# Kernel tuning notes

Hardware: AMD Instinct MI355X
Metric: run time of the kernel (lower is better)

The kernel has to match this reference:

```python
import math
import jax, jax.numpy as jnp
from jax import lax
import numpy as np

LIDAR_MAX_X = 32.0
LIDAR_MAX_Y = 32.0
NQ = 1280  # eval-branch num_queries hardcoded in the torch module


def sineembed(pos, hidden_dim=256):
    # pos (..., 2) -> (..., hidden_dim); DAB-DETR sine embedding
    half = hidden_dim // 2
    dim_t = 10000.0 ** (2.0 * (jnp.arange(half) // 2).astype(jnp.float32) / half)
    scale = 2.0 * math.pi
    px = (pos[..., 0] * scale)[..., None] / dim_t
    py = (pos[..., 1] * scale)[..., None] / dim_t

    def interleave(p):
        s = jnp.stack([jnp.sin(p[..., 0::2]), jnp.cos(p[..., 1::2])], axis=-1)
        return s.reshape(s.shape[:-2] + (-1,))

    return jnp.concatenate([interleave(py), interleave(px)], axis=-1)


def grid_sample_bilinear_zeros(value, grid):
    # value (B,C,H,W); grid (B,Hg,Wg,2) in [-1,1], (x,y) order,
    # bilinear, padding_mode='zeros', align_corners=False
    B, C, H, W = value.shape
    Hg, Wg = grid.shape[1], grid.shape[2]
    gx = ((grid[..., 0] + 1.0) * 0.5 * W - 0.5).reshape(B, -1)
    gy = ((grid[..., 1] + 1.0) * 0.5 * H - 0.5).reshape(B, -1)
    x0 = jnp.floor(gx)
    y0 = jnp.floor(gy)
    wx1 = gx - x0
    wy1 = gy - y0
    vflat = value.reshape(B, C, H * W)

    def gather(ix, iy, w):
        valid = (ix >= 0) & (ix <= W - 1) & (iy >= 0) & (iy <= H - 1)
        ixc = jnp.clip(ix, 0, W - 1).astype(jnp.int32)
        iyc = jnp.clip(iy, 0, H - 1).astype(jnp.int32)
        idx = iyc * W + ixc  # (B,N)
        v = jnp.take_along_axis(vflat, idx[:, None, :], axis=2)  # (B,C,N)
        return v * (w * valid)[:, None, :]

    out = (gather(x0, y0, (1 - wx1) * (1 - wy1))
           + gather(x0 + 1, y0, wx1 * (1 - wy1))
           + gather(x0, y0 + 1, (1 - wx1) * wy1)
           + gather(x0 + 1, y0 + 1, wx1 * wy1))
    return out.reshape(B, C, Hg, Wg)


def setup_inputs() -> dict:
    key = jax.random.key(0)
    ks = jax.random.split(key, 12)
    B, D, Cin, H, W = 8, 256, 64, 200, 200
    return {
        "queries": jax.random.normal(ks[0], (B, NQ, D), jnp.float32),
        "navi_points": jax.random.normal(ks[1], (B, 2), jnp.float32) * 10.0,
        "bev_feature": jax.random.normal(ks[2], (B, Cin, H, W), jnp.float32),
        "spatial_shape": jnp.array([H, W], jnp.int32),
        "point_score": jax.random.uniform(ks[3], (B, 2), jnp.float32),
        "aw_w": jax.random.normal(ks[4], (1, D), jnp.float32) * 0.02,
        "aw_b": jnp.zeros((1,), jnp.float32),
        "aws_w": jax.random.normal(ks[5], (1, D), jnp.float32) * 0.02,
        "aws_b": jnp.zeros((1,), jnp.float32),
        "conv_w": jax.random.normal(ks[6], (256, Cin, 3, 3), jnp.float32) * 0.02,
        "conv_b": jnp.zeros((256,), jnp.float32),
        "out_w": jax.random.normal(ks[7], (D, D), jnp.float32) * 0.02,
        "out_b": jnp.zeros((D,), jnp.float32),
    }


def reference(queries, navi_points, bev_feature, spatial_shape, point_score,
              aw_w, aw_b, aws_w, aws_b, conv_w, conv_b, out_w, out_b):
    B, nq, D = queries.shape
    # eval branch: expand navi_points to (B, 1280, 1, 2)
    pts = jnp.broadcast_to(navi_points.reshape(B, 1, 1, 2), (B, NQ, 1, 2))
    # normalize then swap -> grid (x=pts_y/max_x, y=pts_x/max_y)
    grid = jnp.stack([pts[..., 1] / LIDAR_MAX_X, pts[..., 0] / LIDAR_MAX_Y], axis=-1)

    # attention weights from queries, softmax over num_points (=1)
    aw = jax.nn.softmax(queries @ aw_w.T + aw_b, axis=-1)  # (B,NQ,1)

    # score weights from sine embedding of point_score
    ps = jnp.broadcast_to(point_score.reshape(B, 1, 1, 2), (B, NQ, 1, 2))
    aws = (sineembed(ps) @ aws_w.T + aws_b).reshape(B, NQ, 1)  # (B,NQ,1)

    # value projection: Conv2d 64->256, 3x3, pad 1, ReLU
    value = lax.conv_general_dilated(bev_feature, conv_w, (1, 1), 'SAME',
                                     dimension_numbers=('NCHW', 'OIHW', 'NCHW'))
    value = jax.nn.relu(value + conv_b[None, :, None, None])

    sampled = grid_sample_bilinear_zeros(value, grid)  # (B,256,NQ,1)

    out = (aw[:, None] * sampled * aws[:, None]).sum(axis=-1)  # (B,256,NQ)
    out = out.transpose(0, 2, 1)  # (B,NQ,256)
    out = out @ out_w.T + out_b
    return out + queries  # dropout is identity at inference
```

## Files before the change

kernel.cpp:

```cpp
#include <hip/hip_runtime.h>
#include <math.h>

#define NQ   1280
#define DD   256
#define CIN  64
#define HH   200
#define WW   200
#define BB   8
#define KW   576
#define TPB  256

typedef float floatx4 __attribute__((ext_vector_type(4)));

__device__ __forceinline__ float wave_reduce(float v) {
#pragma unroll
    for (int off = 32; off > 0; off >>= 1) v += __shfl_down(v, off, 64);
    return v;
}

__global__ __launch_bounds__(256) void conv_sample_kernel(
    const float* __restrict__ navi,
    const float* __restrict__ bev,
    const float* __restrict__ pscore,
    const float* __restrict__ aws_w,
    const float* __restrict__ aws_b,
    const float* __restrict__ conv_w,
    const float* __restrict__ conv_b,
    float* __restrict__ s_out,
    float* __restrict__ aws_out)
{
    const int b    = blockIdx.x >> 6;
    const int cgp  = blockIdx.x & 63;
    const int tid  = threadIdx.x;
    const int lane = tid & 63;
    const int wave = tid >> 6;

    __shared__ float win[CIN * 16];
    __shared__ float red[DD];

    float nx = navi[b * 2 + 0];
    float ny = navi[b * 2 + 1];
    float gx = (ny * (1.0f / 32.0f) + 1.0f) * 0.5f * (float)WW - 0.5f;
    float gy = (nx * (1.0f / 32.0f) + 1.0f) * 0.5f * (float)HH - 0.5f;
    float x0f = floorf(gx), y0f = floorf(gy);
    float wx1 = gx - x0f, wy1 = gy - y0f;
    int x0 = (int)x0f, y0 = (int)y0f;

    float cw[4];
    {
        float wx[2] = {1.0f - wx1, wx1};
        float wy[2] = {1.0f - wy1, wy1};
#pragma unroll
        for (int k = 0; k < 4; ++k) {
            int dx = k & 1, dy = k >> 1;
            float ixf = x0f + (float)dx, iyf = y0f + (float)dy;
            bool valid = (ixf >= 0.0f) && (ixf <= (float)(WW - 1)) &&
                         (iyf >= 0.0f) && (iyf <= (float)(HH - 1));
            cw[k] = wx[dx] * wy[dy] * (valid ? 1.0f : 0.0f);
        }
    }

    for (int idx = tid; idx < CIN * 16; idx += TPB) {
        int ci = idx >> 4, pos = idx & 15;
        int yy = y0 - 1 + (pos >> 2);
        int xx = x0 - 1 + (pos & 3);
        float v = 0.0f;
        if (yy >= 0 && yy < HH && xx >= 0 && xx < WW)
            v = bev[((size_t)b * CIN + ci) * (HH * WW) + (size_t)yy * WW + xx];
        win[idx] = v;
    }
    __syncthreads();

    const int c = cgp * 4 + wave;
    const float* wp = conv_w + (size_t)c * KW;
    float a0 = 0.f, a1 = 0.f, a2 = 0.f, a3 = 0.f;
#pragma unroll
    for (int i = 0; i < 9; ++i) {
        int k  = i * 64 + lane;
        int ci = k / 9;
        int r  = k - ci * 9;
        int ky = r / 3;
        int kx = r - ky * 3;
        int base = ci * 16 + ky * 4 + kx;
        float w = wp[k];
        a0 = fmaf(w, win[base],     a0);
        a1 = fmaf(w, win[base + 1], a1);
        a2 = fmaf(w, win[base + 4], a2);
        a3 = fmaf(w, win[base + 5], a3);
    }
    a0 = wave_reduce(a0);
    a1 = wave_reduce(a1);
    a2 = wave_reduce(a2);
    a3 = wave_reduce(a3);
    if (lane == 0) {
        float cb = conv_b[c];
        float v0 = fmaxf(a0 + cb, 0.0f);
        float v1 = fmaxf(a1 + cb, 0.0f);
        float v2 = fmaxf(a2 + cb, 0.0f);
        float v3 = fmaxf(a3 + cb, 0.0f);
        s_out[b * DD + c] = cw[0] * v0 + cw[1] * v1 + cw[2] * v2 + cw[3] * v3;
    }

    if (cgp == 0) {
        float psx = pscore[b * 2 + 0];
        float psy = pscore[b * 2 + 1];
        float p = (tid < 128) ? psy : psx;
        int j = (tid & 127) >> 1;
        float dimt = powf(10000.0f, (float)j * (1.0f / 64.0f));
        float arg = p * 6.283185307179586f / dimt;
        float e = (tid & 1) ? cosf(arg) : sinf(arg);
        red[tid] = e * aws_w[tid];
        __syncthreads();
        for (int off = 128; off > 0; off >>= 1) {
            if (tid < off) red[tid] += red[tid + off];
            __syncthreads();
        }
        if (tid == 0) aws_out[b] = red[0] + aws_b[0];
    }
}

__global__ __launch_bounds__(256) void matvec_kernel(
    const float* __restrict__ out_w,
    const float* __restrict__ out_b,
    const float* __restrict__ s_in,
    const float* __restrict__ aws_in,
    float* __restrict__ t_out)
{
    const int b    = blockIdx.x >> 6;
    const int cgp  = blockIdx.x & 63;
    const int tid  = threadIdx.x;
    const int lane = tid & 63;
    const int wave = tid >> 6;

    __shared__ float s_sh[DD];
    s_sh[tid] = s_in[b * DD + tid];
    __syncthreads();

    const int d = cgp * 4 + wave;
    const float* wp = out_w + (size_t)d * DD;
    float sum = 0.0f;
#pragma unroll
    for (int i = 0; i < 4; ++i)
        sum = fmaf(wp[i * 64 + lane], s_sh[i * 64 + lane], sum);
    sum = wave_reduce(sum);
    if (lane == 0) t_out[b * DD + d] = aws_in[b] * sum + out_b[d];
}

__global__ __launch_bounds__(256) void add_kernel(
    const floatx4* __restrict__ q4,
    const floatx4* __restrict__ t4,
    floatx4* __restrict__ out4)
{
    const int i = blockIdx.x * TPB + threadIdx.x;
    floatx4 v = __builtin_nontemporal_load(&q4[i]);
    const int b  = i / (NQ * DD / 4);
    const int d4 = i & (DD / 4 - 1);
    floatx4 tv = t4[b * (DD / 4) + d4];
    v += tv;
    __builtin_nontemporal_store(v, &out4[i]);
}

extern "C" void kernel_launch(void* const* d_in, const int* in_sizes, int n_in,
                              void* d_out, int out_size, void* d_ws, size_t ws_size,
                              hipStream_t stream) {
    const float* queries = (const float*)d_in[0];
    const float* navi    = (const float*)d_in[1];
    const float* bev     = (const float*)d_in[2];
    const float* pscore  = (const float*)d_in[4];
    const float* aws_w   = (const float*)d_in[7];
    const float* aws_b   = (const float*)d_in[8];
    const float* conv_w  = (const float*)d_in[9];
    const float* conv_b  = (const float*)d_in[10];
    const float* out_w   = (const float*)d_in[11];
    const float* out_b   = (const float*)d_in[12];

    float* s   = (float*)d_ws;
    float* aws = s + BB * DD;
    float* t   = s + BB * DD + 256;

    conv_sample_kernel<<<BB * 64, TPB, 0, stream>>>(navi, bev, pscore, aws_w,
                                                    aws_b, conv_w, conv_b,
                                                    s, aws);
    matvec_kernel<<<BB * 64, TPB, 0, stream>>>(out_w, out_b, s, aws, t);

    const int total4 = BB * NQ * DD / 4;
    add_kernel<<<total4 / TPB, TPB, 0, stream>>>((const floatx4*)queries,
                                                 (const floatx4*)t,
                                                 (floatx4*)d_out);
}
```

Measured before the change: 143.8 us.

## Fuse conv-sample and output matvec into one per-batch kernel

Merges the conv/sampling kernel and the output-projection matvec into a single kernel with one 1024-thread block per batch. Intermediate s and aws values stay in shared memory, removing a launch and a global round trip. The add kernel now uses a 2D grid, so the per-element batch division goes away. The trade-off is parallelism: only 8 blocks run, and each wave loops serially over 16 channels for both the conv and the matvec.

```diff
diff --git a/kernel.cpp b/kernel.cpp
--- a/kernel.cpp
+++ b/kernel.cpp
@@ -18,7 +18,7 @@
     return v;
 }
 
-__global__ __launch_bounds__(256) void conv_sample_kernel(
+__global__ __launch_bounds__(1024) void fused_prep_kernel(
     const float* __restrict__ navi,
     const float* __restrict__ bev,
     const float* __restrict__ pscore,
@@ -26,17 +26,19 @@
     const float* __restrict__ aws_b,
     const float* __restrict__ conv_w,
     const float* __restrict__ conv_b,
-    float* __restrict__ s_out,
-    float* __restrict__ aws_out)
+    const float* __restrict__ out_w,
+    const float* __restrict__ out_b,
+    float* __restrict__ t_out)
 {
-    const int b    = blockIdx.x >> 6;
-    const int cgp  = blockIdx.x & 63;
+    const int b    = blockIdx.x;
     const int tid  = threadIdx.x;
     const int lane = tid & 63;
     const int wave = tid >> 6;
 
     __shared__ float win[CIN * 16];
+    __shared__ float s_sh[DD];
     __shared__ float red[DD];
+    __shared__ float aws_sh;
 
     float nx = navi[b * 2 + 0];
     float ny = navi[b * 2 + 1];
@@ -60,48 +62,49 @@
         }
     }
 
-    for (int idx = tid; idx < CIN * 16; idx += TPB) {
-        int ci = idx >> 4, pos = idx & 15;
+    {
+        int ci = tid >> 4, pos = tid & 15;
         int yy = y0 - 1 + (pos >> 2);
         int xx = x0 - 1 + (pos & 3);
         float v = 0.0f;
         if (yy >= 0 && yy < HH && xx >= 0 && xx < WW)
             v = bev[((size_t)b * CIN + ci) * (HH * WW) + (size_t)yy * WW + xx];
-        win[idx] = v;
+        win[tid] = v;
     }
     __syncthreads();
 
-    const int c = cgp * 4 + wave;
-    const float* wp = conv_w + (size_t)c * KW;
-    float a0 = 0.f, a1 = 0.f, a2 = 0.f, a3 = 0.f;
+    for (int jj = 0; jj < 16; ++jj) {
+        const int c = (wave << 4) + jj;
+        const float* wp = conv_w + (size_t)c * KW;
+        float a0 = 0.f, a1 = 0.f, a2 = 0.f, a3 = 0.f;
 #pragma unroll
-    for (int i = 0; i < 9; ++i) {
-        int k  = i * 64 + lane;
-        int ci = k / 9;
-        int r  = k - ci * 9;
-        int ky = r / 3;
-        int kx = r - ky * 3;
-        int base = ci * 16 + ky * 4 + kx;
-        float w = wp[k];
-        a0 = fmaf(w, win[base],     a0);
-        a1 = fmaf(w, win[base + 1], a1);
-        a2 = fmaf(w, win[base + 4], a2);
-        a3 = fmaf(w, win[base + 5], a3);
-    }
-    a0 = wave_reduce(a0);
-    a1 = wave_reduce(a1);
-    a2 = wave_reduce(a2);
-    a3 = wave_reduce(a3);
-    if (lane == 0) {
-        float cb = conv_b[c];
-        float v0 = fmaxf(a0 + cb, 0.0f);
-        float v1 = fmaxf(a1 + cb, 0.0f);
-        float v2 = fmaxf(a2 + cb, 0.0f);
-        float v3 = fmaxf(a3 + cb, 0.0f);
-        s_out[b * DD + c] = cw[0] * v0 + cw[1] * v1 + cw[2] * v2 + cw[3] * v3;
+        for (int i = 0; i < 9; ++i) {
+            int k  = i * 64 + lane;
+            int ci = k / 9;
+            int r  = k - ci * 9;
+            int ky = r / 3;
+            int kx = r - ky * 3;
+            int base = ci * 16 + ky * 4 + kx;
+            float w = wp[k];
+            a0 = fmaf(w, win[base],     a0);
+            a1 = fmaf(w, win[base + 1], a1);
+            a2 = fmaf(w, win[base + 4], a2);
+            a3 = fmaf(w, win[base + 5], a3);
+        }
+        a0 = wave_reduce(a0);
+        a1 = wave_reduce(a1);
+        a2 = wave_reduce(a2);
+        a3 = wave_reduce(a3);
+        if (lane == 0) {
+            float cb = conv_b[c];
+            s_sh[c] = cw[0] * fmaxf(a0 + cb, 0.0f)
+                    + cw[1] * fmaxf(a1 + cb, 0.0f)
+                    + cw[2] * fmaxf(a2 + cb, 0.0f)
+                    + cw[3] * fmaxf(a3 + cb, 0.0f);
+        }
     }
 
-    if (cgp == 0) {
+    if (tid < DD) {
         float psx = pscore[b * 2 + 0];
         float psy = pscore[b * 2 + 1];
         float p = (tid < 128) ? psy : psx;
@@ -110,40 +113,26 @@
         float arg = p * 6.283185307179586f / dimt;
         float e = (tid & 1) ? cosf(arg) : sinf(arg);
         red[tid] = e * aws_w[tid];
+    }
+    __syncthreads();
+    for (int off = 128; off > 0; off >>= 1) {
+        if (tid < off) red[tid] += red[tid + off];
         __syncthreads();
-        for (int off = 128; off > 0; off >>= 1) {
-            if (tid < off) red[tid] += red[tid + off];
-            __syncthreads();
-        }
-        if (tid == 0) aws_out[b] = red[0] + aws_b[0];
     }
-}
-
-__global__ __launch_bounds__(256) void matvec_kernel(
-    const float* __restrict__ out_w,
-    const float* __restrict__ out_b,
-    const float* __restrict__ s_in,
-    const float* __restrict__ aws_in,
-    float* __restrict__ t_out)
-{
-    const int b    = blockIdx.x >> 6;
-    const int cgp  = blockIdx.x & 63;
-    const int tid  = threadIdx.x;
-    const int lane = tid & 63;
-    const int wave = tid >> 6;
-
-    __shared__ float s_sh[DD];
-    s_sh[tid] = s_in[b * DD + tid];
+    if (tid == 0) aws_sh = red[0] + aws_b[0];
     __syncthreads();
 
-    const int d = cgp * 4 + wave;
-    const float* wp = out_w + (size_t)d * DD;
-    float sum = 0.0f;
+    const float awsv = aws_sh;
+    for (int jj = 0; jj < 16; ++jj) {
+        const int d = (wave << 4) + jj;
+        const float* wp = out_w + (size_t)d * DD;
+        float sum = 0.0f;
 #pragma unroll
-    for (int i = 0; i < 4; ++i)
-        sum = fmaf(wp[i * 64 + lane], s_sh[i * 64 + lane], sum);
-    sum = wave_reduce(sum);
-    if (lane == 0) t_out[b * DD + d] = aws_in[b] * sum + out_b[d];
+        for (int i = 0; i < 4; ++i)
+            sum = fmaf(wp[i * 64 + lane], s_sh[i * 64 + lane], sum);
+        sum = wave_reduce(sum);
+        if (lane == 0) t_out[b * DD + d] = awsv * sum + out_b[d];
+    }
 }
 
 __global__ __launch_bounds__(256) void add_kernel(
@@ -151,11 +140,11 @@
     const floatx4* __restrict__ t4,
     floatx4* __restrict__ out4)
 {
-    const int i = blockIdx.x * TPB + threadIdx.x;
+    const int b  = blockIdx.y;
+    const int il = blockIdx.x * TPB + threadIdx.x;
+    const int i  = b * (NQ * DD / 4) + il;
     floatx4 v = __builtin_nontemporal_load(&q4[i]);
-    const int b  = i / (NQ * DD / 4);
-    const int d4 = i & (DD / 4 - 1);
-    floatx4 tv = t4[b * (DD / 4) + d4];
+    floatx4 tv = t4[b * (DD / 4) + (il & (DD / 4 - 1))];
     v += tv;
     __builtin_nontemporal_store(v, &out4[i]);
 }
@@ -174,17 +163,13 @@
     const float* out_w   = (const float*)d_in[11];
     const float* out_b   = (const float*)d_in[12];
 
-    float* s   = (float*)d_ws;
-    float* aws = s + BB * DD;
-    float* t   = s + BB * DD + 256;
+    float* t = (float*)d_ws;
 
-    conv_sample_kernel<<<BB * 64, TPB, 0, stream>>>(navi, bev, pscore, aws_w,
-                                                    aws_b, conv_w, conv_b,
-                                                    s, aws);
-    matvec_kernel<<<BB * 64, TPB, 0, stream>>>(out_w, out_b, s, aws, t);
+    fused_prep_kernel<<<BB, 1024, 0, stream>>>(navi, bev, pscore, aws_w, aws_b,
+                                               conv_w, conv_b, out_w, out_b, t);
 
-    const int total4 = BB * NQ * DD / 4;
-    add_kernel<<<total4 / TPB, TPB, 0, stream>>>((const floatx4*)queries,
-                                                 (const floatx4*)t,
-                                                 (floatx4*)d_out);
+    dim3 agrid(NQ * DD / 4 / TPB, BB);
+    add_kernel<<<agrid, TPB, 0, stream>>>((const floatx4*)queries,
+                                          (const floatx4*)t,
+                                          (floatx4*)d_out);
 }
```

New measurement: 169.7 us. 18.0% more time.
